# Kernel tuning notes

Hardware: AMD Instinct MI355X
Metric: run time of the kernel (lower is better)

The kernel has to match this reference:

```python
import jax, jax.numpy as jnp
import numpy as np
from jax import lax

B, T_ENC, E = 32, 256, 512
A_RNN, D_RNN, P = 1024, 1024, 256
N_MEL, T_DEC = 80, 800
A_DIM, N_FILT, K = 128, 32, 31
PAD = (K - 1) // 2


def setup_inputs() -> dict:
    key = jax.random.key(0)
    ks = jax.random.split(key, 20)
    rn = lambda k, s, sc=0.02: jax.random.normal(k, s, dtype=jnp.float32) * sc
    return {
        "encoder_outputs": jax.random.normal(ks[0], (B, T_ENC, E), dtype=jnp.float32),
        "decoder_inputs": jax.random.normal(ks[1], (B, N_MEL, T_DEC), dtype=jnp.float32),
        "input_lengths": jax.random.randint(ks[2], (B,), 128, T_ENC + 1),
        "prenet_w1": rn(ks[3], (P, N_MEL)),
        "prenet_w2": rn(ks[4], (P, P)),
        "attn_rnn_Wih": rn(ks[5], (4 * A_RNN, P + E)),
        "attn_rnn_Whh": rn(ks[6], (4 * A_RNN, A_RNN)),
        "attn_rnn_bih": jnp.zeros((4 * A_RNN,), jnp.float32),
        "attn_rnn_bhh": jnp.zeros((4 * A_RNN,), jnp.float32),
        "query_W": rn(ks[7], (A_RNN, A_DIM)),
        "memory_W": rn(ks[8], (E, A_DIM)),
        "v_w": rn(ks[9], (A_DIM,)),
        "loc_conv_W": rn(ks[10], (N_FILT, 2, K)),
        "loc_lin_W": rn(ks[11], (N_FILT, A_DIM)),
        "dec_rnn_Wih": rn(ks[12], (4 * D_RNN, A_RNN + E)),
        "dec_rnn_Whh": rn(ks[13], (4 * D_RNN, D_RNN)),
        "dec_rnn_bih": jnp.zeros((4 * D_RNN,), jnp.float32),
        "dec_rnn_bhh": jnp.zeros((4 * D_RNN,), jnp.float32),
        "proj_W": rn(ks[14], (D_RNN + E, N_MEL)),
        "proj_b": jnp.zeros((N_MEL,), jnp.float32),
        "gate_W": rn(ks[15], (D_RNN + E, 1)),
        "gate_b": jnp.zeros((1,), jnp.float32),
    }


def _lstm_cell(xin, h0, c0, Wih, Whh, bih, bhh):
    # PyTorch LSTMCell gate order: i, f, g, o
    g = xin @ Wih.T + bih + h0 @ Whh.T + bhh
    i, f, gg, o = jnp.split(g, 4, axis=-1)
    c = jax.nn.sigmoid(f) * c0 + jax.nn.sigmoid(i) * jnp.tanh(gg)
    return jax.nn.sigmoid(o) * jnp.tanh(c), c


def _forward(encoder_outputs, decoder_inputs, prenet_w1, prenet_w2,
             attn_rnn_Wih, attn_rnn_Whh, attn_rnn_bih, attn_rnn_bhh,
             query_W, memory_W, v_w, loc_conv_W, loc_lin_W,
             dec_rnn_Wih, dec_rnn_Whh, dec_rnn_bih, dec_rnn_bhh,
             proj_W, proj_b, gate_W, gate_b, input_lengths):
    b, t_enc, e = encoder_outputs.shape
    n_mel = decoder_inputs.shape[1]
    dt = encoder_outputs.dtype

    # parse_decoder_inputs + go frame; keep the T_dec frames actually consumed
    x = jnp.transpose(decoder_inputs, (2, 0, 1))               # [T_dec, B, n_mel]
    go = jnp.zeros((1, b, n_mel), dt)
    x = jnp.concatenate([go, x], 0)[:-1]                       # [T_dec, B, n_mel]

    # Prenet: relu->dropout(p=0.5, always on) x2 (deterministic keys)
    k1, k2 = jax.random.split(jax.random.key(42))
    h = jax.nn.relu(jnp.einsum('tbm,pm->tbp', x, prenet_w1))
    h = h * jax.random.bernoulli(k1, 0.5, h.shape) * 2.0
    h = jax.nn.relu(jnp.einsum('tbp,qp->tbq', h, prenet_w2))
    pre = h * jax.random.bernoulli(k2, 0.5, h.shape) * 2.0     # [T_dec, B, P]

    valid = jnp.arange(t_enc)[None, :] < input_lengths[:, None]  # [B, T_enc]
    pmem = jnp.einsum('bte,ea->bta', encoder_outputs, memory_W)  # processed memory

    def step(carry, xstep):
        ah, ac, dh, dc, ctx, aw, awc = carry
        ah, ac = _lstm_cell(jnp.concatenate([xstep, ctx], -1), ah, ac,
                            attn_rnn_Wih, attn_rnn_Whh, attn_rnn_bih, attn_rnn_bhh)
        # location-sensitive attention (LSA)
        loc = jnp.stack([aw, awc], 1)                           # [B, 2, T_enc]
        lf = lax.conv_general_dilated(loc, loc_conv_W, (1,), [(PAD, PAD)],
                                      dimension_numbers=('NCH', 'OIH', 'NCH'))
        lf = jnp.einsum('bft,fa->bta', lf, loc_lin_W)           # [B, T_enc, A_DIM]
        q = ah @ query_W                                        # [B, A_DIM]
        energies = jnp.tanh(q[:, None, :] + lf + pmem) @ v_w    # [B, T_enc]
        energies = jnp.where(valid, energies, jnp.asarray(-1e9, dt))
        aw = jax.nn.softmax(energies, axis=-1)
        awc = awc + aw
        ctx = jnp.einsum('bt,bte->be', aw, encoder_outputs)
        dh, dc = _lstm_cell(jnp.concatenate([ah, ctx], -1), dh, dc,
                            dec_rnn_Wih, dec_rnn_Whh, dec_rnn_bih, dec_rnn_bhh)
        hc = jnp.concatenate([dh, ctx], -1)
        mel = hc @ proj_W + proj_b                              # [B, n_mel]
        gate = (hc @ gate_W + gate_b)[:, 0]                     # [B]
        return (ah, ac, dh, dc, ctx, aw, awc), (mel, gate, aw)

    z = lambda d: jnp.zeros((b, d), dt)
    carry0 = (z(A_RNN), z(A_RNN), z(D_RNN), z(D_RNN), z(e),
              jnp.zeros((b, t_enc), dt), jnp.zeros((b, t_enc), dt))
    _, (mels, gates, aligns) = lax.scan(step, carry0, pre)

    mel_outputs = jnp.transpose(mels, (1, 2, 0))                # [B, n_mel, T_dec]
    gate_outputs = gates.T                                      # [B, T_dec]
    alignments = jnp.transpose(aligns, (1, 0, 2))               # [B, T_dec, T_enc]
    return mel_outputs, gate_outputs, alignments


def reference(encoder_outputs, decoder_inputs, input_lengths, prenet_w1, prenet_w2,
              attn_rnn_Wih, attn_rnn_Whh, attn_rnn_bih, attn_rnn_bhh,
              query_W, memory_W, v_w, loc_conv_W, loc_lin_W,
              dec_rnn_Wih, dec_rnn_Whh, dec_rnn_bih, dec_rnn_bhh,
              proj_W, proj_b, gate_W, gate_b):
    return _forward(encoder_outputs, decoder_inputs, prenet_w1, prenet_w2,
                    attn_rnn_Wih, attn_rnn_Whh, attn_rnn_bih, attn_rnn_bhh,
                    query_W, memory_W, v_w, loc_conv_W, loc_lin_W,
                    dec_rnn_Wih, dec_rnn_Whh, dec_rnn_bih, dec_rnn_bhh,
                    proj_W, proj_b, gate_W, gate_b, input_lengths)
```

## Files before the change

kernel.cpp:

```cpp
#include <hip/hip_runtime.h>
#include <hip/hip_cooperative_groups.h>
#include <cstdint>
#include <cstddef>

namespace cg = cooperative_groups;

constexpr int B_     = 32;
constexpr int T_ENC  = 256;
constexpr int E_     = 512;
constexpr int A_RNN  = 1024;
constexpr int P_     = 256;
constexpr int N_MEL  = 80;
constexpr int TDEC   = 800;
constexpr int A_DIM  = 128;
constexpr int N_FILT = 32;
constexpr int KCONV  = 31;

constexpr int AH_OFF   = 0;
constexpr int AC_OFF   = 65536;
constexpr int DH_OFF   = 98304;
constexpr int DC_OFF   = 163840;
constexpr int CTX_OFF  = 196608;
constexpr int AW_OFF   = 229376;
constexpr int AWC_OFF  = 237568;
constexpr int EE_OFF   = 245760;
constexpr int STATE_FLOATS = 253952;
constexpr int PRE_OFF  = 253952;
constexpr int PMEM_OFF = 6807552;
constexpr int W1T_OFF  = 7856128;
constexpr int W2T_OFF  = 7876608;

__host__ __device__ inline void tf2x32(uint32_t k0, uint32_t k1, uint32_t& x0, uint32_t& x1) {
  const uint32_t ks2 = k0 ^ k1 ^ 0x1BD11BDAu;
  uint32_t y0 = x0 + k0, y1 = x1 + k1;
#define TFR(r) { y0 += y1; y1 = (y1 << (r)) | (y1 >> (32 - (r))); y1 ^= y0; }
  TFR(13) TFR(15) TFR(26) TFR(6)   y0 += k1;  y1 += ks2 + 1u;
  TFR(17) TFR(29) TFR(16) TFR(24)  y0 += ks2; y1 += k0 + 2u;
  TFR(13) TFR(15) TFR(26) TFR(6)   y0 += k0;  y1 += k1 + 3u;
  TFR(17) TFR(29) TFR(16) TFR(24)  y0 += k1;  y1 += ks2 + 4u;
  TFR(13) TFR(15) TFR(26) TFR(6)   y0 += ks2; y1 += k0 + 5u;
#undef TFR
  x0 = y0; x1 = y1;
}

__device__ inline bool tf_keep(uint32_t ka, uint32_t kb, uint32_t i) {
  uint32_t x0 = 0u, x1 = i;
  tf2x32(ka, kb, x0, x1);
  return (((x0 ^ x1) >> 31) == 0u);
}

__device__ inline float sigm(float x) { return 1.f / (1.f + expf(-x)); }

__global__ __launch_bounds__(256) void transpose_k(const float* __restrict__ src,
                                                   float* __restrict__ dst, int R, int C) {
  int i = blockIdx.x * 256 + threadIdx.x;
  if (i < R * C) { int r = i / C, c = i % C; dst[c * R + r] = src[i]; }
}

__global__ __launch_bounds__(256) void prenet1_kernel(const float* __restrict__ decin,
                                                      const float* __restrict__ w1T,
                                                      float* __restrict__ pre,
                                                      uint32_t ka, uint32_t kb) {
  __shared__ float xs[32][81];
  const int t = blockIdx.x, tid = threadIdx.x;
  for (int f = tid; f < 32 * 80; f += 256) {
    int b = f / 80, m = f % 80;
    xs[b][m] = (t == 0) ? 0.f : decin[b * 64000 + m * 800 + (t - 1)];
  }
  __syncthreads();
  const int p = tid;
  float acc[32];
#pragma unroll
  for (int r = 0; r < 32; ++r) acc[r] = 0.f;
  for (int m = 0; m < 80; ++m) {
    float wv = w1T[m * 256 + p];
#pragma unroll
    for (int r = 0; r < 32; ++r) acc[r] += xs[r][m] * wv;
  }
  float* rowbase = pre + (size_t)t * 32 * 256;
#pragma unroll
  for (int r = 0; r < 32; ++r) {
    float v = fmaxf(acc[r], 0.f);
    uint32_t i = (uint32_t)((t * 32 + r) * 256 + p);
    rowbase[r * 256 + p] = tf_keep(ka, kb, i) ? v * 2.f : 0.f;
  }
}

__global__ __launch_bounds__(256) void prenet2_kernel(const float* __restrict__ w2T,
                                                      float* __restrict__ pre,
                                                      uint32_t ka, uint32_t kb) {
  __shared__ float hs[32][257];
  const int t = blockIdx.x, tid = threadIdx.x;
  float* rowbase = pre + (size_t)t * 32 * 256;
  for (int f = tid; f < 32 * 256; f += 256) {
    int b = f >> 8, k = f & 255;
    hs[b][k] = rowbase[b * 256 + k];
  }
  __syncthreads();
  const int p = tid;
  float acc[32];
#pragma unroll
  for (int r = 0; r < 32; ++r) acc[r] = 0.f;
  for (int k = 0; k < 256; ++k) {
    float wv = w2T[k * 256 + p];
#pragma unroll
    for (int r = 0; r < 32; ++r) acc[r] += hs[r][k] * wv;
  }
#pragma unroll
  for (int r = 0; r < 32; ++r) {
    float v = fmaxf(acc[r], 0.f);
    uint32_t i = (uint32_t)((t * 32 + r) * 256 + p);
    rowbase[r * 256 + p] = tf_keep(ka, kb, i) ? v * 2.f : 0.f;
  }
}

__global__ __launch_bounds__(128) void pmem_kernel(const float* __restrict__ enc,
                                                   const float* __restrict__ memW,
                                                   float* __restrict__ pmem) {
  __shared__ float es[8][513];
  const int b = blockIdx.x >> 5, tg = blockIdx.x & 31, t0 = tg * 8;
  const int tid = threadIdx.x;
  for (int f = tid; f < 8 * 512; f += 128) {
    int rr = f >> 9, e = f & 511;
    es[rr][e] = enc[(size_t)(b * 256 + t0 + rr) * 512 + e];
  }
  __syncthreads();
  float acc[8];
#pragma unroll
  for (int r = 0; r < 8; ++r) acc[r] = 0.f;
  const int a = tid;
  for (int e = 0; e < 512; ++e) {
    float wv = memW[e * 128 + a];
#pragma unroll
    for (int r = 0; r < 8; ++r) acc[r] += es[r][e] * wv;
  }
#pragma unroll
  for (int r = 0; r < 8; ++r) pmem[(size_t)(b * 256 + t0 + r) * 128 + a] = acc[r];
}

struct ScanParams {
  const float* enc; const int* lens;
  const float* aWih; const float* aWhh; const float* abih; const float* abhh;
  const float* qW;   const float* vw;   const float* locW; const float* linW;
  const float* dWih; const float* dWhh; const float* dbih; const float* dbhh;
  const float* pW;   const float* pb;   const float* gW;   const float* gb;
  float* ah; float* ac; float* dh; float* dc; float* ctx; float* aw; float* awc; float* e;
  const float* pre; const float* pmem;
  float* mel_out; float* gate_out; float* align_out;
};

constexpr int SMEM_F = 32 * 132 + 512;

__device__ __forceinline__ void gemm_seg(float4& accv, const float* __restrict__ X, int ldx,
                                         const float* __restrict__ wrow, int len,
                                         int b, int tid, float* xin_s) {
  for (int k0 = 0; k0 < len; k0 += 128) {
    for (int f = tid; f < 32 * 128; f += 512) {
      int bb = f >> 7, kk = f & 127;
      xin_s[bb * 132 + kk] = X[bb * ldx + k0 + kk];
    }
    __syncthreads();
    const float4* w4p = reinterpret_cast<const float4*>(wrow + k0);
    const float4* xr  = reinterpret_cast<const float4*>(xin_s + b * 132);
#pragma unroll
    for (int q = 0; q < 32; ++q) {
      float4 w4 = w4p[q];
      float4 x4 = xr[q];
      accv.x += w4.x * x4.x; accv.y += w4.y * x4.y;
      accv.z += w4.z * x4.z; accv.w += w4.w * x4.w;
    }
    __syncthreads();
  }
}

__device__ void lstm_stage(int blk, int tid,
                           const float* X0, int ld0, int len0,
                           const float* X1, int ld1, int len1,
                           const float* H,
                           const float* Wih, int ldWih, const float* Whh,
                           const float* bih, const float* bhh,
                           float* hout, float* cst, float* smem) {
  const int g = tid >> 7, hh = (tid >> 5) & 3, b = tid & 31;
  const int h0 = blk << 2;
  const int j = (g << 10) + h0 + hh;
  float4 accv = make_float4(0.f, 0.f, 0.f, 0.f);
  float* xin_s = smem;
  gemm_seg(accv, X0, ld0, Wih + (size_t)j * ldWih, len0, b, tid, xin_s);
  gemm_seg(accv, X1, ld1, Wih + (size_t)j * ldWih + len0, len1, b, tid, xin_s);
  gemm_seg(accv, H, 1024, Whh + (size_t)j * 1024, 1024, b, tid, xin_s);
  float acc = ((accv.x + accv.y) + (accv.z + accv.w)) + bih[j] + bhh[j];
  float* gate_s = smem + 32 * 132;
  gate_s[tid] = acc;
  __syncthreads();
  if (tid < 128) {
    const int hh2 = tid >> 5, b2 = tid & 31;
    const float gi = gate_s[(0 * 4 + hh2) * 32 + b2];
    const float gf = gate_s[(1 * 4 + hh2) * 32 + b2];
    const float gg = gate_s[(2 * 4 + hh2) * 32 + b2];
    const float go = gate_s[(3 * 4 + hh2) * 32 + b2];
    const int idx = (b2 << 10) + h0 + hh2;
    float c0 = cst[idx];
    float c = sigm(gf) * c0 + sigm(gi) * tanhf(gg);
    cst[idx] = c;
    hout[idx] = sigm(go) * tanhf(c);
  }
  __syncthreads();
}

__device__ void stage_energies(int blk, int tid, const ScanParams& P, const float* ah_cur,
                               float* smem) {
  const int b = blk >> 3, tile = blk & 7, tt0 = tile * 32;
  float* part = smem;
  float* q_s  = smem + 512;
  float* sLoc = smem + 640;
  float* lf_s = smem + 768;
  float* vw_s = smem + 1824;
  {
    const int js = tid >> 7, a = tid & 127;
    float p = 0.f;
    const float* ahb = ah_cur + b * 1024 + js * 256;
    const float* qWb = P.qW + (js * 256) * 128 + a;
#pragma unroll 4
    for (int jj = 0; jj < 256; ++jj) p += ahb[jj] * qWb[jj * 128];
    part[tid] = p;
  }
  if (tid < 128) vw_s[tid] = P.vw[tid];
  __syncthreads();
  if (tid < 128) q_s[tid] = part[tid] + part[128 + tid] + part[256 + tid] + part[384 + tid];
  else if (tid < 256) {
    int u = tid - 128, c = u >> 6, uu = u & 63;
    int idx = tt0 - 15 + uu;
    float v = 0.f;
    if (idx >= 0 && idx < 256)
      v = (c == 0) ? P.aw[b * 256 + idx] : P.awc[b * 256 + idx];
    sLoc[c * 64 + uu] = v;
  }
  __syncthreads();
#pragma unroll
  for (int oo = 0; oo < 2; ++oo) {
    int o = tid + oo * 512;
    int f = o >> 5, ttl = o & 31;
    float acc = 0.f;
#pragma unroll
    for (int c = 0; c < 2; ++c)
#pragma unroll
      for (int k = 0; k < KCONV; ++k)
        acc += sLoc[c * 64 + ttl + k] * P.locW[f * 62 + c * 31 + k];
    lf_s[f * 33 + ttl] = acc;
  }
  __syncthreads();
  const int ttl = tid >> 4, s = tid & 15;
  const int tt = tt0 + ttl;
  const int lb = P.lens[b];
  float esum = 0.f;
  const float* pmrow = P.pmem + (size_t)(b * 256 + tt) * 128;
#pragma unroll
  for (int r = 0; r < 8; ++r) {
    int a = r * 16 + s;
    float lfa = 0.f;
#pragma unroll
    for (int f = 0; f < 32; ++f) lfa += lf_s[f * 33 + ttl] * P.linW[f * 128 + a];
    float val = tanhf(q_s[a] + lfa + pmrow[a]);
    esum += val * vw_s[a];
  }
#pragma unroll
  for (int m = 1; m < 16; m <<= 1) esum += __shfl_xor(esum, m);
  if (s == 0) P.e[b * 256 + tt] = (tt < lb) ? esum : -1e9f;
}

__device__ void stage_softmax_ctx(int b, int tid, int t, const ScanParams& P,
                                  float* ctxp, float* smem) {
  float* es   = smem;
  float* redm = smem + 256;
  float* reds = smem + 264;
  float ev = (tid < 256) ? P.e[b * 256 + tid] : -3.0e38f;
  float v = ev;
#pragma unroll
  for (int m = 32; m >= 1; m >>= 1) v = fmaxf(v, __shfl_xor(v, m));
  if ((tid & 63) == 0) redm[tid >> 6] = v;
  __syncthreads();
  float mx = redm[0];
#pragma unroll
  for (int i = 1; i < 8; ++i) mx = fmaxf(mx, redm[i]);
  float p = 0.f;
  if (tid < 256) p = expf(ev - mx);
  float sv = p;
#pragma unroll
  for (int m = 32; m >= 1; m >>= 1) sv += __shfl_xor(sv, m);
  if ((tid & 63) == 0) reds[tid >> 6] = sv;
  __syncthreads();
  float denom = reds[0];
#pragma unroll
  for (int i = 1; i < 8; ++i) denom += reds[i];
  const float inv = 1.f / denom;
  if (tid < 256) {
    float awv = p * inv;
    es[tid] = awv;
    P.aw[b * 256 + tid] = awv;
    P.awc[b * 256 + tid] += awv;
    P.align_out[(size_t)b * 204800 + t * 256 + tid] = awv;
  }
  __syncthreads();
  float acc = 0.f;
  const float* encb = P.enc + (size_t)b * 131072 + tid;
#pragma unroll 4
  for (int tt = 0; tt < 256; ++tt) acc += es[tt] * encb[(size_t)tt * 512];
  ctxp[(b << 9) + tid] = acc;
}

__device__ void stage_proj(int b, int tid, int tp, const ScanParams& P,
                           const float* dh_prev, const float* ctx_prev, float* smem) {
  float* hc    = smem;
  float* partm = smem + 1536;
  float* partg = smem + 2016;
  for (int i = tid; i < 1024; i += 512) hc[i] = dh_prev[b * 1024 + i];
  if (tid < 512) hc[1024 + tid] = ctx_prev[(b << 9) + tid];
  __syncthreads();
  if (tid < 480) {
    int ks = tid / 80, m = tid % 80;
    float acc = 0.f;
    const float* pWk = P.pW + (ks * 256) * 80 + m;
    const float* hck = hc + ks * 256;
#pragma unroll 4
    for (int k = 0; k < 256; ++k) acc += hck[k] * pWk[k * 80];
    partm[ks * 80 + m] = acc;
  } else {
    int s = tid - 480;
    float acc = 0.f;
    for (int k = s * 48; k < s * 48 + 48; ++k) acc += hc[k] * P.gW[k];
    partg[s] = acc;
  }
  __syncthreads();
  if (tid < 80) {
    float acc = P.pb[tid];
#pragma unroll
    for (int s = 0; s < 6; ++s) acc += partm[s * 80 + tid];
    P.mel_out[b * 64000 + tid * 800 + tp] = acc;
  }
  if (tid == 511) {
    float acc = P.gb[0];
#pragma unroll
    for (int s = 0; s < 32; ++s) acc += partg[s];
    P.gate_out[b * 800 + tp] = acc;
  }
  __syncthreads();
}

__global__ void __launch_bounds__(512) scan_kernel(ScanParams P) {
  cg::grid_group grid = cg::this_grid();
  const int blk = blockIdx.x, tid = threadIdx.x;
  __shared__ float smem[SMEM_F];

  for (int t = 0; t < TDEC; ++t) {
    const int wp = t & 1, rp = wp ^ 1;
    lstm_stage(blk, tid,
               P.pre + (size_t)t * 8192, 256, 256,
               P.ctx + rp * 16384, 512, 512,
               P.ah + rp * 32768,
               P.aWih, 768, P.aWhh, P.abih, P.abhh,
               P.ah + wp * 32768, P.ac, smem);
    grid.sync();
    stage_energies(blk, tid, P, P.ah + wp * 32768, smem);
    grid.sync();
    if (blk < 32)
      stage_softmax_ctx(blk, tid, t, P, P.ctx + wp * 16384, smem);
    else if (blk < 64 && t > 0)
      stage_proj(blk - 32, tid, t - 1, P, P.dh + rp * 32768, P.ctx + rp * 16384, smem);
    grid.sync();
    lstm_stage(blk, tid,
               P.ah + wp * 32768, 1024, 1024,
               P.ctx + wp * 16384, 512, 512,
               P.dh + rp * 32768,
               P.dWih, 1536, P.dWhh, P.dbih, P.dbhh,
               P.dh + wp * 32768, P.dc, smem);
    grid.sync();
  }
  if (blk >= 32 && blk < 64)
    stage_proj(blk - 32, tid, 799, P, P.dh + 32768, P.ctx + 16384, smem);
}

extern "C" void kernel_launch(void* const* d_in, const int* in_sizes, int n_in,
                              void* d_out, int out_size, void* d_ws, size_t ws_size,
                              hipStream_t stream) {
  (void)in_sizes; (void)n_in; (void)out_size; (void)ws_size;
  const float* enc   = (const float*)d_in[0];
  const float* decin = (const float*)d_in[1];
  const int*   lens  = (const int*)d_in[2];
  const float* w1    = (const float*)d_in[3];
  const float* w2    = (const float*)d_in[4];
  const float* aWih  = (const float*)d_in[5];
  const float* aWhh  = (const float*)d_in[6];
  const float* abih  = (const float*)d_in[7];
  const float* abhh  = (const float*)d_in[8];
  const float* qW    = (const float*)d_in[9];
  const float* memW  = (const float*)d_in[10];
  const float* vw    = (const float*)d_in[11];
  const float* locW  = (const float*)d_in[12];
  const float* linW  = (const float*)d_in[13];
  const float* dWih  = (const float*)d_in[14];
  const float* dWhh  = (const float*)d_in[15];
  const float* dbih  = (const float*)d_in[16];
  const float* dbhh  = (const float*)d_in[17];
  const float* pW    = (const float*)d_in[18];
  const float* pb    = (const float*)d_in[19];
  const float* gW    = (const float*)d_in[20];
  const float* gb    = (const float*)d_in[21];

  float* ws  = (float*)d_ws;
  float* out = (float*)d_out;

  hipMemsetAsync(ws, 0, (size_t)STATE_FLOATS * sizeof(float), stream);

  uint32_t k1a, k1b, k2a, k2b;
  { uint32_t a = 0u, b = 0u; tf2x32(0u, 42u, a, b); k1a = a; k1b = b; }
  { uint32_t a = 0u, b = 1u; tf2x32(0u, 42u, a, b); k2a = a; k2b = b; }

  transpose_k<<<dim3((256 * 80 + 255) / 256), dim3(256), 0, stream>>>(w1, ws + W1T_OFF, 256, 80);
  transpose_k<<<dim3((256 * 256 + 255) / 256), dim3(256), 0, stream>>>(w2, ws + W2T_OFF, 256, 256);
  prenet1_kernel<<<dim3(800), dim3(256), 0, stream>>>(decin, ws + W1T_OFF, ws + PRE_OFF, k1a, k1b);
  prenet2_kernel<<<dim3(800), dim3(256), 0, stream>>>(ws + W2T_OFF, ws + PRE_OFF, k2a, k2b);
  pmem_kernel<<<dim3(1024), dim3(128), 0, stream>>>(enc, memW, ws + PMEM_OFF);

  ScanParams prm;
  prm.enc = enc; prm.lens = lens;
  prm.aWih = aWih; prm.aWhh = aWhh; prm.abih = abih; prm.abhh = abhh;
  prm.qW = qW; prm.vw = vw; prm.locW = locW; prm.linW = linW;
  prm.dWih = dWih; prm.dWhh = dWhh; prm.dbih = dbih; prm.dbhh = dbhh;
  prm.pW = pW; prm.pb = pb; prm.gW = gW; prm.gb = gb;
  prm.ah = ws + AH_OFF; prm.ac = ws + AC_OFF;
  prm.dh = ws + DH_OFF; prm.dc = ws + DC_OFF;
  prm.ctx = ws + CTX_OFF; prm.aw = ws + AW_OFF; prm.awc = ws + AWC_OFF; prm.e = ws + EE_OFF;
  prm.pre = ws + PRE_OFF; prm.pmem = ws + PMEM_OFF;
  prm.mel_out = out; prm.gate_out = out + 2048000; prm.align_out = out + 2073600;

  void* kargs[] = { (void*)&prm };
  hipLaunchCooperativeKernel(scan_kernel, dim3(256), dim3(512), kargs, 0, stream);
}
```

Before: 423.9 ms.

## Fuse attention energies and softmax into one stage, prefetch-pipeline LSTM GEMMs

Merges the energy and softmax/context stages into a single per-batch attention stage run by 32 blocks. This removes one grid-wide sync per decoder step and the global round trip of the energy buffer. The LSTM gate GEMM is rewritten with 256-wide chunks, register prefetch of the next chunk's inputs and weights, each thread computing 4 rows x 8 batches, and a butterfly shuffle reduction. Blocks grow to 1024 threads, and the location linear weight is pre-transposed. The risk is that only 32 blocks do all the attention work (loc conv over all 256 positions), which may serialize that stage, and register pressure is higher at 1024 threads.

```diff
diff --git a/kernel.cpp b/kernel.cpp
--- a/kernel.cpp
+++ b/kernel.cpp
@@ -5,15 +5,7 @@
 
 namespace cg = cooperative_groups;
 
-constexpr int B_     = 32;
-constexpr int T_ENC  = 256;
-constexpr int E_     = 512;
-constexpr int A_RNN  = 1024;
-constexpr int P_     = 256;
-constexpr int N_MEL  = 80;
 constexpr int TDEC   = 800;
-constexpr int A_DIM  = 128;
-constexpr int N_FILT = 32;
 constexpr int KCONV  = 31;
 
 constexpr int AH_OFF   = 0;
@@ -29,6 +21,7 @@
 constexpr int PMEM_OFF = 6807552;
 constexpr int W1T_OFF  = 7856128;
 constexpr int W2T_OFF  = 7876608;
+constexpr int LINT_OFF = 7942144;
 
 __host__ __device__ inline void tf2x32(uint32_t k0, uint32_t k1, uint32_t& x0, uint32_t& x1) {
   const uint32_t ks2 = k0 ^ k1 ^ 0x1BD11BDAu;
@@ -141,171 +134,270 @@
 struct ScanParams {
   const float* enc; const int* lens;
   const float* aWih; const float* aWhh; const float* abih; const float* abhh;
-  const float* qW;   const float* vw;   const float* locW; const float* linW;
+  const float* qW;   const float* vw;   const float* locW; const float* linT;
   const float* dWih; const float* dWhh; const float* dbih; const float* dbhh;
   const float* pW;   const float* pb;   const float* gW;   const float* gb;
-  float* ah; float* ac; float* dh; float* dc; float* ctx; float* aw; float* awc; float* e;
+  float* ah; float* ac; float* dh; float* dc; float* ctx; float* aw; float* awc;
   const float* pre; const float* pmem;
   float* mel_out; float* gate_out; float* align_out;
 };
 
-constexpr int SMEM_F = 32 * 132 + 512;
-
-__device__ __forceinline__ void gemm_seg(float4& accv, const float* __restrict__ X, int ldx,
-                                         const float* __restrict__ wrow, int len,
-                                         int b, int tid, float* xin_s) {
-  for (int k0 = 0; k0 < len; k0 += 128) {
-    for (int f = tid; f < 32 * 128; f += 512) {
-      int bb = f >> 7, kk = f & 127;
-      xin_s[bb * 132 + kk] = X[bb * ldx + k0 + kk];
+constexpr int SMEM_F = 11456;
+
+struct XW { const float* x; int ldx; const float* w; int ldw; };
+
+__device__ __forceinline__ void stage_load(const XW& ch, float4* sreg, int tid) {
+#pragma unroll
+  for (int u = 0; u < 2; ++u) {
+    int f4 = tid * 2 + u;
+    int bs = f4 >> 6;
+    int kk = (f4 & 63) * 4;
+    sreg[u] = *(const float4*)(ch.x + (size_t)bs * ch.ldx + kk);
+  }
+}
+__device__ __forceinline__ void stage_store(const float4* sreg, float* dst, int tid) {
+#pragma unroll
+  for (int u = 0; u < 2; ++u) {
+    int f4 = tid * 2 + u;
+    int bs = f4 >> 6;
+    int kk = (f4 & 63) * 4;
+    *(float4*)(dst + bs * 256 + kk) = sreg[u];
+  }
+}
+
+template <typename F>
+__device__ __forceinline__ void lstm_core(int blk, int tid, int nc, F getc,
+                                          const float* bih, const float* bhh,
+                                          float* hout, float* cst, float* smem) {
+  const int lane = tid & 63;
+  const int bg = (tid >> 6) & 3;
+  const int jg = tid >> 8;
+  const int b0 = bg * 8;
+  const int hb = blk * 4;
+  float* xs = smem;
+  float* gate_s = smem + 8192;
+
+  float acc[4][8];
+#pragma unroll
+  for (int rr = 0; rr < 4; ++rr) {
+    float bv = (lane == 0) ? (bih[jg * 1024 + hb + rr] + bhh[jg * 1024 + hb + rr]) : 0.f;
+#pragma unroll
+    for (int bb = 0; bb < 8; ++bb) acc[rr][bb] = bv;
+  }
+
+  float4 sreg[2];
+  {
+    XW c0 = getc(0);
+    stage_load(c0, sreg, tid);
+    stage_store(sreg, xs, tid);
+  }
+  float4 wc[4];
+  {
+    XW c0 = getc(0);
+#pragma unroll
+    for (int rr = 0; rr < 4; ++rr)
+      wc[rr] = *(const float4*)(c0.w + (size_t)(jg * 1024 + hb + rr) * c0.ldw + lane * 4);
+  }
+  __syncthreads();
+
+  for (int c = 0; c < nc; ++c) {
+    float4 wn[4];
+    const bool more = (c + 1 < nc);
+    if (more) {
+      XW cn = getc(c + 1);
+      stage_load(cn, sreg, tid);
+#pragma unroll
+      for (int rr = 0; rr < 4; ++rr)
+        wn[rr] = *(const float4*)(cn.w + (size_t)(jg * 1024 + hb + rr) * cn.ldw + lane * 4);
+    }
+#pragma unroll
+    for (int bb = 0; bb < 8; ++bb) {
+      float4 x4 = *(const float4*)(xs + (b0 + bb) * 256 + lane * 4);
+#pragma unroll
+      for (int rr = 0; rr < 4; ++rr) {
+        acc[rr][bb] = fmaf(wc[rr].x, x4.x, acc[rr][bb]);
+        acc[rr][bb] = fmaf(wc[rr].y, x4.y, acc[rr][bb]);
+        acc[rr][bb] = fmaf(wc[rr].z, x4.z, acc[rr][bb]);
+        acc[rr][bb] = fmaf(wc[rr].w, x4.w, acc[rr][bb]);
+      }
     }
     __syncthreads();
-    const float4* w4p = reinterpret_cast<const float4*>(wrow + k0);
-    const float4* xr  = reinterpret_cast<const float4*>(xin_s + b * 132);
-#pragma unroll
-    for (int q = 0; q < 32; ++q) {
-      float4 w4 = w4p[q];
-      float4 x4 = xr[q];
-      accv.x += w4.x * x4.x; accv.y += w4.y * x4.y;
-      accv.z += w4.z * x4.z; accv.w += w4.w * x4.w;
-    }
-    __syncthreads();
-  }
-}
-
-__device__ void lstm_stage(int blk, int tid,
-                           const float* X0, int ld0, int len0,
-                           const float* X1, int ld1, int len1,
-                           const float* H,
-                           const float* Wih, int ldWih, const float* Whh,
-                           const float* bih, const float* bhh,
-                           float* hout, float* cst, float* smem) {
-  const int g = tid >> 7, hh = (tid >> 5) & 3, b = tid & 31;
-  const int h0 = blk << 2;
-  const int j = (g << 10) + h0 + hh;
-  float4 accv = make_float4(0.f, 0.f, 0.f, 0.f);
-  float* xin_s = smem;
-  gemm_seg(accv, X0, ld0, Wih + (size_t)j * ldWih, len0, b, tid, xin_s);
-  gemm_seg(accv, X1, ld1, Wih + (size_t)j * ldWih + len0, len1, b, tid, xin_s);
-  gemm_seg(accv, H, 1024, Whh + (size_t)j * 1024, 1024, b, tid, xin_s);
-  float acc = ((accv.x + accv.y) + (accv.z + accv.w)) + bih[j] + bhh[j];
-  float* gate_s = smem + 32 * 132;
-  gate_s[tid] = acc;
+    if (more) {
+      stage_store(sreg, xs, tid);
+#pragma unroll
+      for (int rr = 0; rr < 4; ++rr) wc[rr] = wn[rr];
+      __syncthreads();
+    }
+  }
+
+  float v[32];
+#pragma unroll
+  for (int rr = 0; rr < 4; ++rr)
+#pragma unroll
+    for (int bb = 0; bb < 8; ++bb) v[rr * 8 + bb] = acc[rr][bb];
+#pragma unroll
+  for (int s = 0; s < 5; ++s) {
+    const int d = 32 >> s;
+    const int half = 32 >> (s + 1);
+    const bool up = (lane & d) != 0;
+#pragma unroll
+    for (int i = 0; i < 16; ++i) {
+      if (i < half) {
+        float send = up ? v[i] : v[i + half];
+        float got = __shfl_xor(send, d);
+        v[i] = (up ? v[i + half] : v[i]) + got;
+      }
+    }
+  }
+  v[0] += __shfl_xor(v[0], 1);
+  if ((lane & 1) == 0) {
+    int p = (lane >> 1) & 31;
+    int rr = p >> 3, bb = p & 7;
+    gate_s[(jg * 4 + rr) * 33 + (b0 + bb)] = v[0];
+  }
   __syncthreads();
   if (tid < 128) {
-    const int hh2 = tid >> 5, b2 = tid & 31;
-    const float gi = gate_s[(0 * 4 + hh2) * 32 + b2];
-    const float gf = gate_s[(1 * 4 + hh2) * 32 + b2];
-    const float gg = gate_s[(2 * 4 + hh2) * 32 + b2];
-    const float go = gate_s[(3 * 4 + hh2) * 32 + b2];
-    const int idx = (b2 << 10) + h0 + hh2;
-    float c0 = cst[idx];
-    float c = sigm(gf) * c0 + sigm(gi) * tanhf(gg);
-    cst[idx] = c;
-    hout[idx] = sigm(go) * tanhf(c);
-  }
-  __syncthreads();
-}
-
-__device__ void stage_energies(int blk, int tid, const ScanParams& P, const float* ah_cur,
-                               float* smem) {
-  const int b = blk >> 3, tile = blk & 7, tt0 = tile * 32;
+    int hl = tid >> 5, b = tid & 31;
+    float gi = gate_s[(0 + hl) * 33 + b];
+    float gf = gate_s[(4 + hl) * 33 + b];
+    float gg = gate_s[(8 + hl) * 33 + b];
+    float go = gate_s[(12 + hl) * 33 + b];
+    int idx = b * 1024 + hb + hl;
+    float c0v = cst[idx];
+    float cn = sigm(gf) * c0v + sigm(gi) * tanhf(gg);
+    cst[idx] = cn;
+    hout[idx] = sigm(go) * tanhf(cn);
+  }
+}
+
+__device__ void stage_attn(int b, int tid, int t, const ScanParams& P,
+                           const float* ah_cur, float* ctx_out, float* smem) {
   float* part = smem;
-  float* q_s  = smem + 512;
-  float* sLoc = smem + 640;
-  float* lf_s = smem + 768;
-  float* vw_s = smem + 1824;
+  float* sLoc = smem + 1024;
+  float* q_s  = smem + 1600;
+  float* vw_s = smem + 1728;
+  float* red  = smem + 1856;
+  float* aw_s = smem + 1888;
+  float* cpart= smem + 2144;
+  float* lf_s = smem + 3200;
   {
     const int js = tid >> 7, a = tid & 127;
-    float p = 0.f;
-    const float* ahb = ah_cur + b * 1024 + js * 256;
-    const float* qWb = P.qW + (js * 256) * 128 + a;
+    const float* ahb = ah_cur + b * 1024 + js * 128;
+    const float* qp = P.qW + (size_t)(js * 128) * 128 + a;
+    float p0 = 0.f, p1 = 0.f, p2 = 0.f, p3 = 0.f;
+    for (int j = 0; j < 128; j += 4) {
+      p0 += ahb[j] * qp[(size_t)j * 128];
+      p1 += ahb[j + 1] * qp[(size_t)(j + 1) * 128];
+      p2 += ahb[j + 2] * qp[(size_t)(j + 2) * 128];
+      p3 += ahb[j + 3] * qp[(size_t)(j + 3) * 128];
+    }
+    part[tid] = (p0 + p1) + (p2 + p3);
+  }
+  if (tid < 572) {
+    int c = tid / 286, i = tid % 286;
+    int src = i - 15;
+    float vv = 0.f;
+    if (src >= 0 && src < 256) vv = (c == 0 ? P.aw : P.awc)[b * 256 + src];
+    sLoc[c * 286 + i] = vv;
+  } else if (tid < 700) {
+    vw_s[tid - 572] = P.vw[tid - 572];
+  }
+  __syncthreads();
+  if (tid < 128) {
+    float q = 0.f;
+#pragma unroll
+    for (int js = 0; js < 8; ++js) q += part[js * 128 + tid];
+    q_s[tid] = q;
+  }
+  {
+    const int f = tid >> 5, tg = tid & 31;
+    float accL[8];
+#pragma unroll
+    for (int i = 0; i < 8; ++i) accL[i] = 0.f;
+    const float* wf = P.locW + f * 62;
+#pragma unroll
+    for (int c = 0; c < 2; ++c)
+#pragma unroll
+      for (int k = 0; k < KCONV; ++k) {
+        float wv = wf[c * 31 + k];
+        const float* sl = sLoc + c * 286 + tg * 8 + k;
+#pragma unroll
+        for (int i = 0; i < 8; ++i) accL[i] += sl[i] * wv;
+      }
+#pragma unroll
+    for (int i = 0; i < 8; ++i) lf_s[f * 258 + tg * 8 + i] = accL[i];
+  }
+  __syncthreads();
+  {
+    const int tt = tid >> 2, aq = tid & 3;
+    float lfv[32];
+#pragma unroll
+    for (int f = 0; f < 32; ++f) lfv[f] = lf_s[f * 258 + tt];
+    const float* pm = P.pmem + (size_t)(b * 256 + tt) * 128;
+    float ep = 0.f;
 #pragma unroll 4
-    for (int jj = 0; jj < 256; ++jj) p += ahb[jj] * qWb[jj * 128];
-    part[tid] = p;
-  }
-  if (tid < 128) vw_s[tid] = P.vw[tid];
-  __syncthreads();
-  if (tid < 128) q_s[tid] = part[tid] + part[128 + tid] + part[256 + tid] + part[384 + tid];
-  else if (tid < 256) {
-    int u = tid - 128, c = u >> 6, uu = u & 63;
-    int idx = tt0 - 15 + uu;
-    float v = 0.f;
-    if (idx >= 0 && idx < 256)
-      v = (c == 0) ? P.aw[b * 256 + idx] : P.awc[b * 256 + idx];
-    sLoc[c * 64 + uu] = v;
-  }
-  __syncthreads();
-#pragma unroll
-  for (int oo = 0; oo < 2; ++oo) {
-    int o = tid + oo * 512;
-    int f = o >> 5, ttl = o & 31;
-    float acc = 0.f;
-#pragma unroll
-    for (int c = 0; c < 2; ++c)
-#pragma unroll
-      for (int k = 0; k < KCONV; ++k)
-        acc += sLoc[c * 64 + ttl + k] * P.locW[f * 62 + c * 31 + k];
-    lf_s[f * 33 + ttl] = acc;
-  }
-  __syncthreads();
-  const int ttl = tid >> 4, s = tid & 15;
-  const int tt = tt0 + ttl;
-  const int lb = P.lens[b];
-  float esum = 0.f;
-  const float* pmrow = P.pmem + (size_t)(b * 256 + tt) * 128;
-#pragma unroll
-  for (int r = 0; r < 8; ++r) {
-    int a = r * 16 + s;
-    float lfa = 0.f;
-#pragma unroll
-    for (int f = 0; f < 32; ++f) lfa += lf_s[f * 33 + ttl] * P.linW[f * 128 + a];
-    float val = tanhf(q_s[a] + lfa + pmrow[a]);
-    esum += val * vw_s[a];
-  }
-#pragma unroll
-  for (int m = 1; m < 16; m <<= 1) esum += __shfl_xor(esum, m);
-  if (s == 0) P.e[b * 256 + tt] = (tt < lb) ? esum : -1e9f;
-}
-
-__device__ void stage_softmax_ctx(int b, int tid, int t, const ScanParams& P,
-                                  float* ctxp, float* smem) {
-  float* es   = smem;
-  float* redm = smem + 256;
-  float* reds = smem + 264;
-  float ev = (tid < 256) ? P.e[b * 256 + tid] : -3.0e38f;
-  float v = ev;
-#pragma unroll
-  for (int m = 32; m >= 1; m >>= 1) v = fmaxf(v, __shfl_xor(v, m));
-  if ((tid & 63) == 0) redm[tid >> 6] = v;
-  __syncthreads();
-  float mx = redm[0];
-#pragma unroll
-  for (int i = 1; i < 8; ++i) mx = fmaxf(mx, redm[i]);
-  float p = 0.f;
-  if (tid < 256) p = expf(ev - mx);
-  float sv = p;
-#pragma unroll
-  for (int m = 32; m >= 1; m >>= 1) sv += __shfl_xor(sv, m);
-  if ((tid & 63) == 0) reds[tid >> 6] = sv;
-  __syncthreads();
-  float denom = reds[0];
-#pragma unroll
-  for (int i = 1; i < 8; ++i) denom += reds[i];
-  const float inv = 1.f / denom;
+    for (int ai = 0; ai < 32; ++ai) {
+      int a = aq * 32 + ai;
+      const float4* lt = (const float4*)(P.linT + a * 32);
+      float lfa = 0.f;
+#pragma unroll
+      for (int u = 0; u < 8; ++u) {
+        float4 l4 = lt[u];
+        lfa += l4.x * lfv[u * 4] + l4.y * lfv[u * 4 + 1] + l4.z * lfv[u * 4 + 2] + l4.w * lfv[u * 4 + 3];
+      }
+      float val = tanhf(q_s[a] + lfa + pm[a]);
+      ep += val * vw_s[a];
+    }
+    part[tid] = ep;
+  }
+  __syncthreads();
+  const int len_b = P.lens[b];
   if (tid < 256) {
-    float awv = p * inv;
-    es[tid] = awv;
+    float e = part[tid * 4] + part[tid * 4 + 1] + part[tid * 4 + 2] + part[tid * 4 + 3];
+    e = (tid < len_b) ? e : -1e9f;
+    aw_s[tid] = e;
+  }
+  __syncthreads();
+  if (tid < 64) {
+    float m0 = fmaxf(fmaxf(aw_s[tid], aw_s[64 + tid]), fmaxf(aw_s[128 + tid], aw_s[192 + tid]));
+#pragma unroll
+    for (int m = 32; m >= 1; m >>= 1) m0 = fmaxf(m0, __shfl_xor(m0, m));
+    if (tid == 0) red[0] = m0;
+  }
+  __syncthreads();
+  const float mx = red[0];
+  if (tid < 256) part[tid] = expf(aw_s[tid] - mx);
+  __syncthreads();
+  if (tid < 64) {
+    float s0 = part[tid] + part[64 + tid] + part[128 + tid] + part[192 + tid];
+#pragma unroll
+    for (int m = 32; m >= 1; m >>= 1) s0 += __shfl_xor(s0, m);
+    if (tid == 0) red[1] = s0;
+  }
+  __syncthreads();
+  const float inv = 1.f / red[1];
+  if (tid < 256) {
+    float awv = part[tid] * inv;
+    aw_s[tid] = awv;
     P.aw[b * 256 + tid] = awv;
     P.awc[b * 256 + tid] += awv;
-    P.align_out[(size_t)b * 204800 + t * 256 + tid] = awv;
-  }
-  __syncthreads();
-  float acc = 0.f;
-  const float* encb = P.enc + (size_t)b * 131072 + tid;
-#pragma unroll 4
-  for (int tt = 0; tt < 256; ++tt) acc += es[tt] * encb[(size_t)tt * 512];
-  ctxp[(b << 9) + tid] = acc;
+    P.align_out[(size_t)b * 204800 + (size_t)t * 256 + tid] = awv;
+  }
+  __syncthreads();
+  {
+    const int ee = tid & 511, hf = tid >> 9;
+    const float* encb = P.enc + (size_t)b * 131072 + (size_t)hf * 128 * 512 + ee;
+    float a0 = 0.f, a1 = 0.f, a2 = 0.f, a3 = 0.f;
+    for (int tt = 0; tt < 128; tt += 4) {
+      a0 += aw_s[hf * 128 + tt] * encb[(size_t)tt * 512];
+      a1 += aw_s[hf * 128 + tt + 1] * encb[(size_t)(tt + 1) * 512];
+      a2 += aw_s[hf * 128 + tt + 2] * encb[(size_t)(tt + 2) * 512];
+      a3 += aw_s[hf * 128 + tt + 3] * encb[(size_t)(tt + 3) * 512];
+    }
+    cpart[hf * 512 + ee] = (a0 + a1) + (a2 + a3);
+  }
+  __syncthreads();
+  if (tid < 512) ctx_out[b * 512 + tid] = cpart[tid] + cpart[512 + tid];
 }
 
 __device__ void stage_proj(int b, int tid, int tp, const ScanParams& P,
@@ -313,18 +405,22 @@
   float* hc    = smem;
   float* partm = smem + 1536;
   float* partg = smem + 2016;
-  for (int i = tid; i < 1024; i += 512) hc[i] = dh_prev[b * 1024 + i];
-  if (tid < 512) hc[1024 + tid] = ctx_prev[(b << 9) + tid];
+  for (int i = tid; i < 1536; i += 1024)
+    hc[i] = (i < 1024) ? dh_prev[b * 1024 + i] : ctx_prev[b * 512 + (i - 1024)];
   __syncthreads();
   if (tid < 480) {
     int ks = tid / 80, m = tid % 80;
-    float acc = 0.f;
-    const float* pWk = P.pW + (ks * 256) * 80 + m;
+    const float* pWk = P.pW + (size_t)(ks * 256) * 80 + m;
     const float* hck = hc + ks * 256;
-#pragma unroll 4
-    for (int k = 0; k < 256; ++k) acc += hck[k] * pWk[k * 80];
-    partm[ks * 80 + m] = acc;
-  } else {
+    float a0 = 0.f, a1 = 0.f, a2 = 0.f, a3 = 0.f;
+    for (int k = 0; k < 256; k += 4) {
+      a0 += hck[k] * pWk[(size_t)k * 80];
+      a1 += hck[k + 1] * pWk[(size_t)(k + 1) * 80];
+      a2 += hck[k + 2] * pWk[(size_t)(k + 2) * 80];
+      a3 += hck[k + 3] * pWk[(size_t)(k + 3) * 80];
+    }
+    partm[ks * 80 + m] = (a0 + a1) + (a2 + a3);
+  } else if (tid < 512) {
     int s = tid - 480;
     float acc = 0.f;
     for (int k = s * 48; k < s * 48 + 48; ++k) acc += hc[k] * P.gW[k];
@@ -343,36 +439,49 @@
     for (int s = 0; s < 32; ++s) acc += partg[s];
     P.gate_out[b * 800 + tp] = acc;
   }
-  __syncthreads();
-}
-
-__global__ void __launch_bounds__(512) scan_kernel(ScanParams P) {
+}
+
+__global__ void __launch_bounds__(1024, 4) scan_kernel(ScanParams P) {
   cg::grid_group grid = cg::this_grid();
   const int blk = blockIdx.x, tid = threadIdx.x;
   __shared__ float smem[SMEM_F];
 
   for (int t = 0; t < TDEC; ++t) {
     const int wp = t & 1, rp = wp ^ 1;
-    lstm_stage(blk, tid,
-               P.pre + (size_t)t * 8192, 256, 256,
-               P.ctx + rp * 16384, 512, 512,
-               P.ah + rp * 32768,
-               P.aWih, 768, P.aWhh, P.abih, P.abhh,
-               P.ah + wp * 32768, P.ac, smem);
-    grid.sync();
-    stage_energies(blk, tid, P, P.ah + wp * 32768, smem);
+    {
+      const float* pre_t = P.pre + (size_t)t * 8192;
+      const float* ctx_r = P.ctx + rp * 16384;
+      const float* ah_r  = P.ah + rp * 32768;
+      const ScanParams& Q = P;
+      auto getc1 = [&](int c) -> XW {
+        XW r;
+        if (c == 0)      { r.x = pre_t;               r.ldx = 256;  r.w = Q.aWih;                      r.ldw = 768; }
+        else if (c <= 2) { r.x = ctx_r + (c - 1) * 256; r.ldx = 512; r.w = Q.aWih + 256 + (c - 1) * 256; r.ldw = 768; }
+        else             { r.x = ah_r + (c - 3) * 256;  r.ldx = 1024; r.w = Q.aWhh + (c - 3) * 256;      r.ldw = 1024; }
+        return r;
+      };
+      lstm_core(blk, tid, 7, getc1, P.abih, P.abhh, P.ah + wp * 32768, P.ac, smem);
+    }
     grid.sync();
     if (blk < 32)
-      stage_softmax_ctx(blk, tid, t, P, P.ctx + wp * 16384, smem);
+      stage_attn(blk, tid, t, P, P.ah + wp * 32768, P.ctx + wp * 16384, smem);
     else if (blk < 64 && t > 0)
       stage_proj(blk - 32, tid, t - 1, P, P.dh + rp * 32768, P.ctx + rp * 16384, smem);
     grid.sync();
-    lstm_stage(blk, tid,
-               P.ah + wp * 32768, 1024, 1024,
-               P.ctx + wp * 16384, 512, 512,
-               P.dh + rp * 32768,
-               P.dWih, 1536, P.dWhh, P.dbih, P.dbhh,
-               P.dh + wp * 32768, P.dc, smem);
+    {
+      const float* ah_w  = P.ah + wp * 32768;
+      const float* ctx_w = P.ctx + wp * 16384;
+      const float* dh_r  = P.dh + rp * 32768;
+      const ScanParams& Q = P;
+      auto getc2 = [&](int c) -> XW {
+        XW r;
+        if (c <= 3)      { r.x = ah_w + c * 256;        r.ldx = 1024; r.w = Q.dWih + c * 256;            r.ldw = 1536; }
+        else if (c <= 5) { r.x = ctx_w + (c - 4) * 256; r.ldx = 512;  r.w = Q.dWih + 1024 + (c - 4) * 256; r.ldw = 1536; }
+        else             { r.x = dh_r + (c - 6) * 256;  r.ldx = 1024; r.w = Q.dWhh + (c - 6) * 256;       r.ldw = 1024; }
+        return r;
+      };
+      lstm_core(blk, tid, 10, getc2, P.dbih, P.dbhh, P.dh + wp * 32768, P.dc, smem);
+    }
     grid.sync();
   }
   if (blk >= 32 && blk < 64)
@@ -417,6 +526,7 @@
 
   transpose_k<<<dim3((256 * 80 + 255) / 256), dim3(256), 0, stream>>>(w1, ws + W1T_OFF, 256, 80);
   transpose_k<<<dim3((256 * 256 + 255) / 256), dim3(256), 0, stream>>>(w2, ws + W2T_OFF, 256, 256);
+  transpose_k<<<dim3((32 * 128 + 255) / 256), dim3(256), 0, stream>>>(linW, ws + LINT_OFF, 32, 128);
   prenet1_kernel<<<dim3(800), dim3(256), 0, stream>>>(decin, ws + W1T_OFF, ws + PRE_OFF, k1a, k1b);
   prenet2_kernel<<<dim3(800), dim3(256), 0, stream>>>(ws + W2T_OFF, ws + PRE_OFF, k2a, k2b);
   pmem_kernel<<<dim3(1024), dim3(128), 0, stream>>>(enc, memW, ws + PMEM_OFF);
@@ -424,15 +534,15 @@
   ScanParams prm;
   prm.enc = enc; prm.lens = lens;
   prm.aWih = aWih; prm.aWhh = aWhh; prm.abih = abih; prm.abhh = abhh;
-  prm.qW = qW; prm.vw = vw; prm.locW = locW; prm.linW = linW;
+  prm.qW = qW; prm.vw = vw; prm.locW = locW; prm.linT = ws + LINT_OFF;
   prm.dWih = dWih; prm.dWhh = dWhh; prm.dbih = dbih; prm.dbhh = dbhh;
   prm.pW = pW; prm.pb = pb; prm.gW = gW; prm.gb = gb;
   prm.ah = ws + AH_OFF; prm.ac = ws + AC_OFF;
   prm.dh = ws + DH_OFF; prm.dc = ws + DC_OFF;
-  prm.ctx = ws + CTX_OFF; prm.aw = ws + AW_OFF; prm.awc = ws + AWC_OFF; prm.e = ws + EE_OFF;
+  prm.ctx = ws + CTX_OFF; prm.aw = ws + AW_OFF; prm.awc = ws + AWC_OFF;
   prm.pre = ws + PRE_OFF; prm.pmem = ws + PMEM_OFF;
   prm.mel_out = out; prm.gate_out = out + 2048000; prm.align_out = out + 2073600;
 
   void* kargs[] = { (void*)&prm };
-  hipLaunchCooperativeKernel(scan_kernel, dim3(256), dim3(512), kargs, 0, stream);
-}
+  hipLaunchCooperativeKernel(scan_kernel, dim3(256), dim3(1024), kargs, 0, stream);
+}
```

Result: faster. 360.5 ms (-15.0%).
